# Kernel optimization log

Hardware: AMD Instinct MI355X
Metric: run time of the kernel (lower is better)

Reference implementation:

```python
import jax, jax.numpy as jnp
import numpy as np

NEG = -10000.0
T, K = 65536, 512


def setup_inputs() -> dict:
    key = jax.random.key(0)
    k1, k2 = jax.random.split(key)
    feats = jax.random.normal(k1, (T, K), dtype=jnp.float32)
    transitions = jax.random.normal(k2, (K, K), dtype=jnp.float32)
    # constraints from __init__: never transition INTO start tag (col 0),
    # never transition OUT of stop tag row (row 1)
    transitions = transitions.at[:, 0].set(NEG).at[1, :].set(NEG)
    return {"feats": feats, "transitions": transitions}


def reference(feats, transitions):
    K_ = transitions.shape[0]
    init = jnp.full((K_,), NEG, dtype=feats.dtype).at[0].set(0.0)

    def step(fv, feat):
        # scores[next, prev] = fv[prev] + transitions[next, prev]
        scores = fv[None, :] + transitions
        bp = jnp.argmax(scores, axis=1).astype(jnp.int32)   # backpointers [K]
        fv_new = jnp.max(scores, axis=1) + feat             # viterbi vars + emission
        return fv_new, bp

    fv, bptrs = jax.lax.scan(step, init, feats)  # bptrs: [T, K]

    terminal = fv + transitions[1]
    best = jnp.argmax(terminal).astype(jnp.int32)
    path_score = terminal[best]

    # backtrack: outs[t] = bptrs[t][path[t]] = path[t-1]; outs[0] is the start tag (0)
    def back(tag, bp):
        nt = bp[tag]
        return nt, nt

    _, outs = jax.lax.scan(back, best, bptrs, reverse=True)
    best_path = jnp.concatenate([outs[1:], best[None]])  # [T], tags per timestep
    return path_score, best_path
```

## Files before the change

### kernel.cpp

```cpp
#include <hip/hip_runtime.h>
#include <cstdint>
#include <cstddef>

#define TT 65536
#define KK 512
#define NEGV (-10000.0f)
#define SEG 256
#define NSEG 256

typedef unsigned short u16;
typedef unsigned int   u32;
typedef unsigned long long u64;

__device__ __forceinline__ float u2f(u32 b){ union{u32 u; float f;} x; x.u=b; return x.f; }
__device__ __forceinline__ u32 f2u(float f){ union{u32 u; float f;} x; x.f=f; return x.u; }

__global__ __launch_bounds__(512)
void sort_rows(const float* __restrict__ trans, u64* __restrict__ svpT,
               u64* __restrict__ svpR)
{
    __shared__ u64 s[KK];
    const int n = blockIdx.x, i = threadIdx.x;
    float x = trans[n*KK + i];
    u32 b = f2u(x);
    u32 ord = (b & 0x80000000u) ? ~b : (b | 0x80000000u);
    s[i] = ((u64)(~ord) << 16) | (u32)i;
    __syncthreads();
    for (int k = 2; k <= KK; k <<= 1){
        for (int j = k >> 1; j > 0; j >>= 1){
            int ixj = i ^ j;
            if (ixj > i){
                u64 a = s[i], c = s[ixj];
                bool up = ((i & k) == 0);
                if ((a > c) == up){ s[i] = c; s[ixj] = a; }
            }
            __syncthreads();
        }
    }
    u64 key = s[i];
    u32 p    = (u32)(key & 0xFFFFu);
    u32 ordv = ~(u32)(key >> 16);
    u32 bits = (ordv & 0x80000000u) ? (ordv ^ 0x80000000u) : ~ordv;
    u64 ent = ((u64)p << 32) | bits;
    svpT[(size_t)i*KK + n] = ent;
    svpR[(size_t)n*KK + i] = ent;
}

__global__ __launch_bounds__(512)
void transpose_k(const float* __restrict__ t, float* __restrict__ tt)
{
    const int c = blockIdx.x, r = threadIdx.x;
    tt[(size_t)c*KK + r] = t[(size_t)r*KK + c];
}

__global__ __launch_bounds__(512)
void fv_scan(const float* __restrict__ feats,
             const u64* __restrict__ svpT,
             const u64* __restrict__ svpR,
             const float* __restrict__ transT,
             float* __restrict__ fvBound,
             float* __restrict__ fmArr,
             float* __restrict__ outScore, int* __restrict__ bestOut)
{
    __shared__ float fvb[2][KK];
    __shared__ float wmaxS[2][8];
    __shared__ u64  bmS[4][8];
    __shared__ u32  cntS[4][8];
    __shared__ u64  bandE[KK + 8];
    __shared__ float rv[KK];
    __shared__ int   ri[KK];

    const int i = threadIdx.x, lane = i & 63, wv = i >> 6;
    const u64 laneLT = (1ull << lane) - 1ull;

    float cV[16]; int cP[16];
#pragma unroll
    for (int k = 0; k < 16; ++k){
        u64 e = svpT[(size_t)k*KK + i];
        cV[k] = u2f((u32)e); cP[k] = (int)(e >> 32);
    }

    float fv_i = fmaxf(NEGV, NEGV + cV[0]) + feats[i];
    fvBound[i] = fv_i;
    float featCur = feats[(size_t)KK + i];

#define VMAX8(k0) { \
    float f0=fvc[cP[k0]],     f1=fvc[cP[(k0)+1]], f2=fvc[cP[(k0)+2]], f3=fvc[cP[(k0)+3]]; \
    float f4=fvc[cP[(k0)+4]], f5=fvc[cP[(k0)+5]], f6=fvc[cP[(k0)+6]], f7=fvc[cP[(k0)+7]]; \
    float m0=fmaxf(f0+cV[k0],     f1+cV[(k0)+1]), m1=fmaxf(f2+cV[(k0)+2], f3+cV[(k0)+3]); \
    float m2=fmaxf(f4+cV[(k0)+4], f5+cV[(k0)+5]), m3=fmaxf(f6+cV[(k0)+6], f7+cV[(k0)+7]); \
    best = fmaxf(best, fmaxf(fmaxf(m0,m1), fmaxf(m2,m3))); }

    for (int t = 1; t < TT; ++t){
        const int cur = t & 1;

        fvb[cur][i] = fv_i;
        float wm = fv_i;
#pragma unroll
        for (int o = 32; o > 0; o >>= 1) wm = fmaxf(wm, __shfl_xor(wm, o, 64));
        if (lane == 0) wmaxS[cur][wv] = wm;
        __syncthreads();
        float fm = wmaxS[cur][0];
#pragma unroll
        for (int w = 1; w < 8; ++w) fm = fmaxf(fm, wmaxS[cur][w]);
        if (i == 0) fmArr[t] = fm;
        const float e0 = fm-0.5f, e1 = fm-1.0f, e2 = fm-1.5f, e3 = fm-2.0f;
        u64 q0 = __ballot(fv_i > e0), q1 = __ballot(fv_i > e1);
        u64 q2 = __ballot(fv_i > e2), q3 = __ballot(fv_i > e3);
        if (lane == 0){
            u64 b0 = q0, b1 = q1&~q0, b2 = q2&~q1, b3 = q3&~q2;
            bmS[0][wv]=b0; cntS[0][wv]=(u32)__builtin_popcountll(b0);
            bmS[1][wv]=b1; cntS[1][wv]=(u32)__builtin_popcountll(b1);
            bmS[2][wv]=b2; cntS[2][wv]=(u32)__builtin_popcountll(b2);
            bmS[3][wv]=b3; cntS[3][wv]=(u32)__builtin_popcountll(b3);
        }

        const float* fvc = fvb[cur];
        float featNxt = __builtin_nontemporal_load(
            &feats[(size_t)(t+1 < TT ? t+1 : t)*KK + i]);
        float best = -3.0e38f;
        VMAX8(0) VMAX8(8)
        __syncthreads();

        u32 tot0=0, tot1=0, tot2=0, tot3=0;
#pragma unroll
        for (int w = 0; w < 8; ++w){
            tot0 += cntS[0][w]; tot1 += cntS[1][w];
            tot2 += cntS[2][w]; tot3 += cntS[3][w];
        }
        int b_i = (fv_i > e0) ? 0 : (fv_i > e1) ? 1 : (fv_i > e2) ? 2 :
                  (fv_i > e3) ? 3 : 4;
        if (b_i < 4){
            u32 off = (b_i > 0 ? tot0 : 0u) + (b_i > 1 ? tot1 : 0u) +
                      (b_i > 2 ? tot2 : 0u);
#pragma unroll
            for (int w = 0; w < 8; ++w) off += (w < wv) ? cntS[b_i][w] : 0u;
            off += (u32)__builtin_popcountll(bmS[b_i][wv] & laneLT);
            bandE[off] = ((u64)f2u(fv_i) << 32) | (u32)i;
        }
        u32 totAll = tot0 + tot1 + tot2 + tot3;
        if (i < 8) bandE[totAll + i] = ((u64)f2u(-1.0e30f) << 32);
        int s0 = __builtin_amdgcn_readfirstlane((int)tot0);
        int s1 = __builtin_amdgcn_readfirstlane((int)tot1);
        int s2 = __builtin_amdgcn_readfirstlane((int)tot2);
        int s3 = __builtin_amdgcn_readfirstlane((int)tot3);
        __syncthreads();

        bool done = false;
        int base = 0;
#pragma unroll
        for (int b = 0; b < 4; ++b){
            const int  cntb = (b==0)?s0:(b==1)?s1:(b==2)?s2:s3;
            const float edge = (b==0)?e0:(b==1)?e1:(b==2)?e2:e3;
            if (__any(!done)){
                if (!done && cntb > 0){
                    for (int u = 0; u < cntb; u += 8){
                        const int jj = base + u;
                        u64 E0=bandE[jj],   E1=bandE[jj+1], E2=bandE[jj+2], E3=bandE[jj+3];
                        u64 E4=bandE[jj+4], E5=bandE[jj+5], E6=bandE[jj+6], E7=bandE[jj+7];
                        int p0=(int)(E0&0xFFFFu), p1=(int)(E1&0xFFFFu);
                        int p2=(int)(E2&0xFFFFu), p3=(int)(E3&0xFFFFu);
                        int p4=(int)(E4&0xFFFFu), p5=(int)(E5&0xFFFFu);
                        int p6=(int)(E6&0xFFFFu), p7=(int)(E7&0xFFFFu);
                        float t0=transT[(size_t)p0*KK+i], t1=transT[(size_t)p1*KK+i];
                        float t2=transT[(size_t)p2*KK+i], t3=transT[(size_t)p3*KK+i];
                        float t4=transT[(size_t)p4*KK+i], t5=transT[(size_t)p5*KK+i];
                        float t6=transT[(size_t)p6*KK+i], t7=transT[(size_t)p7*KK+i];
                        float a0=u2f((u32)(E0>>32))+t0, a1=u2f((u32)(E1>>32))+t1;
                        float a2=u2f((u32)(E2>>32))+t2, a3=u2f((u32)(E3>>32))+t3;
                        float a4=u2f((u32)(E4>>32))+t4, a5=u2f((u32)(E5>>32))+t5;
                        float a6=u2f((u32)(E6>>32))+t6, a7=u2f((u32)(E7>>32))+t7;
                        best = fmaxf(best,
                               fmaxf(fmaxf(fmaxf(a0,a1),fmaxf(a2,a3)),
                                     fmaxf(fmaxf(a4,a5),fmaxf(a6,a7))));
                    }
                }
                done = done || (edge + cV[15] <= best);
            }
            base += cntb;
        }

        u64 pend = __ballot(!done);
        while (pend){
            int r = (int)__ffsll((unsigned long long)pend) - 1;
            pend &= pend - 1;
            const int row = (wv << 6) + r;
            float bestR = __shfl(best, r, 64);
            int rk = 16 + lane;
            for (;;){
                float vv = -1.0e30f, sc = -1.0e30f;
                if (rk < KK){
                    u64 e = svpR[(size_t)row*KK + rk];
                    vv = u2f((u32)e);
                    sc = fvc[(int)(e >> 32)] + vv;
                }
                float m = sc;
#pragma unroll
                for (int o = 32; o > 0; o >>= 1) m = fmaxf(m, __shfl_xor(m, o, 64));
                bestR = fmaxf(bestR, m);
                float vl = __shfl(vv, 63, 64);
                if (e3 + vl <= bestR) break;
                rk += 64;
            }
            if (lane == r) best = bestR;
        }

        fv_i = best + featCur;
        featCur = featNxt;
        if ((t & (SEG-1)) == 0)
            fvBound[(size_t)(t >> 8)*KK + i] = fv_i;
    }
#undef VMAX8

    float tv = fv_i + NEGV;
    rv[i] = tv; ri[i] = i;
    __syncthreads();
    for (int s2 = 256; s2 > 0; s2 >>= 1){
        if (i < s2){
            float v2 = rv[i+s2]; int i2 = ri[i+s2];
            if (v2 > rv[i] || (v2 == rv[i] && i2 < ri[i])){ rv[i] = v2; ri[i] = i2; }
        }
        __syncthreads();
    }
    if (i == 0){ outScore[0] = rv[0]; *bestOut = ri[0]; }
}

__global__ __launch_bounds__(512)
void bp_fill(const float* __restrict__ feats,
             const u64* __restrict__ svpT,
             const float* __restrict__ fvBound,
             const float* __restrict__ fmArr,
             u16* __restrict__ bp)
{
    __shared__ float fvb[2][KK];
    __shared__ u64  r1S[2][8];
    const int i = threadIdx.x, lane = i & 63, wv = i >> 6;
    const int s = blockIdx.x;
    const int t0 = s*SEG + 1;
    const int tEnd = (s == NSEG-1) ? (TT-1) : (s*SEG + SEG);

    float fv_i = fvBound[(size_t)s*KK + i];
    float featC = feats[(size_t)t0*KK + i];

#define TAKE(p_, val_) { float _val=(val_); int _p=(p_); \
    bool _tk = (_val > best) || (_val == best && _p < barg); \
    best = _tk ? _val : best; barg = _tk ? _p : barg; }

    for (int t = t0; t <= tEnd; ++t){
        const int cur = t & 1;
        fvb[cur][i] = fv_i;
        float sc1 = fv_i + NEGV;
        u32 bb = f2u(sc1);
        u32 od = (bb & 0x80000000u) ? ~bb : (bb | 0x80000000u);
        u64 key = ((u64)od << 32) | (u32)(KK - 1 - i);
#pragma unroll
        for (int o = 32; o > 0; o >>= 1){
            u64 ok = __shfl_xor(key, o, 64);
            key = (ok > key) ? ok : key;
        }
        if (lane == 0) r1S[cur][wv] = key;
        float featN = (t < tEnd) ? feats[(size_t)(t+1)*KK + i] : 0.0f;
        __syncthreads();
        const float fm = fmArr[t];
        const float* fvc = fvb[cur];
        float best; int barg;
        if (i == 1){
            u64 kk = r1S[cur][0];
#pragma unroll
            for (int w = 1; w < 8; ++w){ u64 o2 = r1S[cur][w]; kk = (o2 > kk) ? o2 : kk; }
            barg = (KK - 1) - (int)(u32)kk;
            best = fm + NEGV;
        } else {
            best = -3.0e38f; barg = 0;
            for (int kb = 0; kb < KK; kb += 8){
                const u64* sp = &svpT[(size_t)kb*KK + i];
                u64 E0 = sp[0];          u64 E1 = sp[(size_t)KK];
                u64 E2 = sp[(size_t)2*KK]; u64 E3 = sp[(size_t)3*KK];
                u64 E4 = sp[(size_t)4*KK]; u64 E5 = sp[(size_t)5*KK];
                u64 E6 = sp[(size_t)6*KK]; u64 E7 = sp[(size_t)7*KK];
                int p0=(int)(E0>>32), p1=(int)(E1>>32), p2=(int)(E2>>32), p3=(int)(E3>>32);
                int p4=(int)(E4>>32), p5=(int)(E5>>32), p6=(int)(E6>>32), p7=(int)(E7>>32);
                TAKE(p0, fvc[p0] + u2f((u32)E0)); TAKE(p1, fvc[p1] + u2f((u32)E1));
                TAKE(p2, fvc[p2] + u2f((u32)E2)); TAKE(p3, fvc[p3] + u2f((u32)E3));
                TAKE(p4, fvc[p4] + u2f((u32)E4)); TAKE(p5, fvc[p5] + u2f((u32)E5));
                TAKE(p6, fvc[p6] + u2f((u32)E6)); TAKE(p7, fvc[p7] + u2f((u32)E7));
                float vlast = u2f((u32)E7);
                if (fm + vlast < best) break;
            }
        }
        __builtin_nontemporal_store((u16)barg, &bp[(size_t)t*KK + i]);
        fv_i = best + featC;
        featC = featN;
    }
#undef TAKE
}

__global__ __launch_bounds__(512)
void bt_maps(const u16* __restrict__ bp, u16* __restrict__ maps)
{
    const int s = blockIdx.x, e = threadIdx.x;
    const int tEnd = (s == NSEG-1) ? (TT-1) : (s+1)*SEG;
    const int tLow = s*SEG;
    int cur = e;
    for (int t = tEnd; t > tLow; --t) cur = (int)bp[(size_t)t*KK + cur];
    maps[s*KK + e] = (u16)cur;
}

__global__ void bt_boundaries(const u16* __restrict__ maps, const int* __restrict__ bestP,
                              int* __restrict__ btag)
{
    if (threadIdx.x != 0 || blockIdx.x != 0) return;
    int cur = *bestP;
    for (int s = NSEG-1; s >= 0; --s){
        cur = (int)maps[s*KK + cur];
        btag[s] = cur;
    }
}

__global__ void bt_decode(const u16* __restrict__ bp, const int* __restrict__ btag,
                          const int* __restrict__ bestP, float* __restrict__ outPath)
{
    const int s = blockIdx.x;
    if (threadIdx.x != 0) return;
    int tEnd, cur;
    if (s == NSEG-1){ tEnd = TT-1; cur = *bestP; outPath[TT-1] = (float)cur; }
    else            { tEnd = (s+1)*SEG; cur = btag[s+1]; }
    for (int t = tEnd; t > s*SEG; --t){
        cur = (int)bp[(size_t)t*KK + cur];
        outPath[t-1] = (float)cur;
    }
}

extern "C" void kernel_launch(void* const* d_in, const int* in_sizes, int n_in,
                              void* d_out, int out_size, void* d_ws, size_t ws_size,
                              hipStream_t stream)
{
    (void)in_sizes; (void)n_in; (void)out_size; (void)ws_size;
    const float* feats = (const float*)d_in[0];
    const float* trans = (const float*)d_in[1];
    float* out = (float*)d_out;

    char* ws = (char*)d_ws;
    size_t off = 0;
    u16*   bp     = (u16*)(ws + off);   off += (size_t)TT*KK*sizeof(u16);
    u64*   svpT   = (u64*)(ws + off);   off += (size_t)KK*KK*sizeof(u64);
    u64*   svpR   = (u64*)(ws + off);   off += (size_t)KK*KK*sizeof(u64);
    float* transT = (float*)(ws + off); off += (size_t)KK*KK*sizeof(float);
    float* fvBound= (float*)(ws + off); off += (size_t)NSEG*KK*sizeof(float);
    float* fmArr  = (float*)(ws + off); off += (size_t)TT*sizeof(float);
    u16*   maps   = (u16*)(ws + off);   off += (size_t)NSEG*KK*sizeof(u16);
    int*   btag   = (int*)(ws + off);   off += (size_t)(NSEG+8)*sizeof(int);
    int*   bestP  = (int*)(ws + off);

    hipLaunchKernelGGL(sort_rows,     dim3(KK),   dim3(512), 0, stream, trans, svpT, svpR);
    hipLaunchKernelGGL(transpose_k,   dim3(KK),   dim3(512), 0, stream, trans, transT);
    hipLaunchKernelGGL(fv_scan,       dim3(1),    dim3(512), 0, stream, feats, svpT, svpR,
                       transT, fvBound, fmArr, out, bestP);
    hipLaunchKernelGGL(bp_fill,       dim3(NSEG), dim3(512), 0, stream, feats, svpT,
                       fvBound, fmArr, bp);
    hipLaunchKernelGGL(bt_maps,       dim3(NSEG), dim3(512), 0, stream, bp, maps);
    hipLaunchKernelGGL(bt_boundaries, dim3(1),    dim3(64),  0, stream, maps, bestP, btag);
    hipLaunchKernelGGL(bt_decode,     dim3(NSEG), dim3(64),  0, stream, bp, btag, bestP, out + 1);
}
```

Measured before the change: 297.4 ms.

## Replace band compaction with per-wave bitmask iteration and add argmax-candidate seeding

Drops the shared-memory prefix-sum compaction of band candidates and the extra barrier it needed. Each band is now walked directly from per-wave ballot bitmasks using ffs. The band count grows from four to eight, widening the pruning range before falling back to the slow sorted-row scan. Each wave's argmax previous state (packed into a 64-bit key) is also used to seed the running best with its transition column, which tightens the early-exit bound. The costs are serialized bitmask loops with scalar readfirstlane, eight extra global loads of transT per step, and possibly more band iterations.

```diff
diff --git a/kernel.cpp b/kernel.cpp
--- a/kernel.cpp
+++ b/kernel.cpp
@@ -63,15 +63,12 @@
              float* __restrict__ outScore, int* __restrict__ bestOut)
 {
     __shared__ float fvb[2][KK];
-    __shared__ float wmaxS[2][8];
-    __shared__ u64  bmS[4][8];
-    __shared__ u32  cntS[4][8];
-    __shared__ u64  bandE[KK + 8];
+    __shared__ u64  wmaxS[2][8];
+    __shared__ u64  bmS[8][8];
     __shared__ float rv[KK];
     __shared__ int   ri[KK];
 
     const int i = threadIdx.x, lane = i & 63, wv = i >> 6;
-    const u64 laneLT = (1ull << lane) - 1ull;
 
     float cV[16]; int cP[16];
 #pragma unroll
@@ -79,6 +76,7 @@
         u64 e = svpT[(size_t)k*KK + i];
         cV[k] = u2f((u32)e); cP[k] = (int)(e >> 32);
     }
+    const float cv15 = cV[15];
 
     float fv_i = fmaxf(NEGV, NEGV + cV[0]) + feats[i];
     fvBound[i] = fv_i;
@@ -95,24 +93,48 @@
         const int cur = t & 1;
 
         fvb[cur][i] = fv_i;
-        float wm = fv_i;
-#pragma unroll
-        for (int o = 32; o > 0; o >>= 1) wm = fmaxf(wm, __shfl_xor(wm, o, 64));
-        if (lane == 0) wmaxS[cur][wv] = wm;
+        {
+            u32 ob = f2u(fv_i);
+            ob = (ob & 0x80000000u) ? ~ob : (ob | 0x80000000u);
+            u64 key = ((u64)ob << 32) | (u32)i;
+#pragma unroll
+            for (int o = 32; o > 0; o >>= 1){
+                u64 ok = __shfl_xor(key, o, 64);
+                key = (ok > key) ? ok : key;
+            }
+            if (lane == 0) wmaxS[cur][wv] = key;
+        }
         __syncthreads();
-        float fm = wmaxS[cur][0];
-#pragma unroll
-        for (int w = 1; w < 8; ++w) fm = fmaxf(fm, wmaxS[cur][w]);
+
+        float wmv[8], pfv[8];
+#pragma unroll
+        for (int w = 0; w < 8; ++w){
+            u64 kw = wmaxS[cur][w];
+            u32 ov = (u32)(kw >> 32);
+            u32 bits = (ov & 0x80000000u) ? (ov ^ 0x80000000u) : ~ov;
+            wmv[w] = u2f(bits);
+            int pw = __builtin_amdgcn_readfirstlane((int)(u32)kw);
+            pfv[w] = transT[(size_t)pw*KK + i];
+        }
+        float fm = wmv[0];
+#pragma unroll
+        for (int w = 1; w < 8; ++w) fm = fmaxf(fm, wmv[w]);
         if (i == 0) fmArr[t] = fm;
+
         const float e0 = fm-0.5f, e1 = fm-1.0f, e2 = fm-1.5f, e3 = fm-2.0f;
-        u64 q0 = __ballot(fv_i > e0), q1 = __ballot(fv_i > e1);
-        u64 q2 = __ballot(fv_i > e2), q3 = __ballot(fv_i > e3);
-        if (lane == 0){
-            u64 b0 = q0, b1 = q1&~q0, b2 = q2&~q1, b3 = q3&~q2;
-            bmS[0][wv]=b0; cntS[0][wv]=(u32)__builtin_popcountll(b0);
-            bmS[1][wv]=b1; cntS[1][wv]=(u32)__builtin_popcountll(b1);
-            bmS[2][wv]=b2; cntS[2][wv]=(u32)__builtin_popcountll(b2);
-            bmS[3][wv]=b3; cntS[3][wv]=(u32)__builtin_popcountll(b3);
+        const float e4 = fm-2.5f, e5 = fm-3.0f, e6 = fm-3.5f, e7 = fm-4.0f;
+        {
+            u64 q0 = __ballot(fv_i > e0), q1 = __ballot(fv_i > e1);
+            u64 q2 = __ballot(fv_i > e2), q3 = __ballot(fv_i > e3);
+            u64 q4 = __ballot(fv_i > e4), q5 = __ballot(fv_i > e5);
+            u64 q6 = __ballot(fv_i > e6), q7 = __ballot(fv_i > e7);
+            if (lane < 8){
+                u64 mb = (lane==0)? q0      : (lane==1)? (q1&~q0) :
+                         (lane==2)? (q2&~q1): (lane==3)? (q3&~q2) :
+                         (lane==4)? (q4&~q3): (lane==5)? (q5&~q4) :
+                         (lane==6)? (q6&~q5):            (q7&~q6);
+                bmS[lane][wv] = mb;
+            }
         }
 
         const float* fvc = fvb[cur];
@@ -120,64 +142,41 @@
             &feats[(size_t)(t+1 < TT ? t+1 : t)*KK + i]);
         float best = -3.0e38f;
         VMAX8(0) VMAX8(8)
+#pragma unroll
+        for (int w = 0; w < 8; ++w) best = fmaxf(best, wmv[w] + pfv[w]);
         __syncthreads();
 
-        u32 tot0=0, tot1=0, tot2=0, tot3=0;
-#pragma unroll
-        for (int w = 0; w < 8; ++w){
-            tot0 += cntS[0][w]; tot1 += cntS[1][w];
-            tot2 += cntS[2][w]; tot3 += cntS[3][w];
-        }
-        int b_i = (fv_i > e0) ? 0 : (fv_i > e1) ? 1 : (fv_i > e2) ? 2 :
-                  (fv_i > e3) ? 3 : 4;
-        if (b_i < 4){
-            u32 off = (b_i > 0 ? tot0 : 0u) + (b_i > 1 ? tot1 : 0u) +
-                      (b_i > 2 ? tot2 : 0u);
-#pragma unroll
-            for (int w = 0; w < 8; ++w) off += (w < wv) ? cntS[b_i][w] : 0u;
-            off += (u32)__builtin_popcountll(bmS[b_i][wv] & laneLT);
-            bandE[off] = ((u64)f2u(fv_i) << 32) | (u32)i;
-        }
-        u32 totAll = tot0 + tot1 + tot2 + tot3;
-        if (i < 8) bandE[totAll + i] = ((u64)f2u(-1.0e30f) << 32);
-        int s0 = __builtin_amdgcn_readfirstlane((int)tot0);
-        int s1 = __builtin_amdgcn_readfirstlane((int)tot1);
-        int s2 = __builtin_amdgcn_readfirstlane((int)tot2);
-        int s3 = __builtin_amdgcn_readfirstlane((int)tot3);
-        __syncthreads();
-
         bool done = false;
-        int base = 0;
-#pragma unroll
-        for (int b = 0; b < 4; ++b){
-            const int  cntb = (b==0)?s0:(b==1)?s1:(b==2)?s2:s3;
-            const float edge = (b==0)?e0:(b==1)?e1:(b==2)?e2:e3;
-            if (__any(!done)){
-                if (!done && cntb > 0){
-                    for (int u = 0; u < cntb; u += 8){
-                        const int jj = base + u;
-                        u64 E0=bandE[jj],   E1=bandE[jj+1], E2=bandE[jj+2], E3=bandE[jj+3];
-                        u64 E4=bandE[jj+4], E5=bandE[jj+5], E6=bandE[jj+6], E7=bandE[jj+7];
-                        int p0=(int)(E0&0xFFFFu), p1=(int)(E1&0xFFFFu);
-                        int p2=(int)(E2&0xFFFFu), p3=(int)(E3&0xFFFFu);
-                        int p4=(int)(E4&0xFFFFu), p5=(int)(E5&0xFFFFu);
-                        int p6=(int)(E6&0xFFFFu), p7=(int)(E7&0xFFFFu);
-                        float t0=transT[(size_t)p0*KK+i], t1=transT[(size_t)p1*KK+i];
-                        float t2=transT[(size_t)p2*KK+i], t3=transT[(size_t)p3*KK+i];
-                        float t4=transT[(size_t)p4*KK+i], t5=transT[(size_t)p5*KK+i];
-                        float t6=transT[(size_t)p6*KK+i], t7=transT[(size_t)p7*KK+i];
-                        float a0=u2f((u32)(E0>>32))+t0, a1=u2f((u32)(E1>>32))+t1;
-                        float a2=u2f((u32)(E2>>32))+t2, a3=u2f((u32)(E3>>32))+t3;
-                        float a4=u2f((u32)(E4>>32))+t4, a5=u2f((u32)(E5>>32))+t5;
-                        float a6=u2f((u32)(E6>>32))+t6, a7=u2f((u32)(E7>>32))+t7;
-                        best = fmaxf(best,
-                               fmaxf(fmaxf(fmaxf(a0,a1),fmaxf(a2,a3)),
-                                     fmaxf(fmaxf(a4,a5),fmaxf(a6,a7))));
+#pragma unroll 1
+        for (int b = 0; b < 8; ++b){
+            if (!__any(!done)) break;
+            const float edge = fm - 0.5f*(float)(b+1);
+            if (!done){
+#pragma unroll 1
+                for (int w = 0; w < 8; ++w){
+                    u64 mraw = bmS[b][w];
+                    u32 mlo = __builtin_amdgcn_readfirstlane((u32)mraw);
+                    u32 mhi = __builtin_amdgcn_readfirstlane((u32)(mraw >> 32));
+                    u64 m = ((u64)mhi << 32) | mlo;
+                    const int pb0 = w << 6;
+                    while (m){
+                        int a0 = (int)__ffsll(m) - 1;  u64 mm = m & (m-1);
+                        int a1 = mm ? (int)__ffsll(mm)-1 : a0;  mm &= (mm-1);
+                        int a2 = mm ? (int)__ffsll(mm)-1 : a0;  mm &= (mm-1);
+                        int a3 = mm ? (int)__ffsll(mm)-1 : a0;  mm &= (mm-1);
+                        m = mm;
+                        const int P0 = pb0+a0, P1 = pb0+a1, P2 = pb0+a2, P3 = pb0+a3;
+                        float f0 = fvc[P0], f1 = fvc[P1], f2 = fvc[P2], f3 = fvc[P3];
+                        float t0 = transT[(size_t)P0*KK + i];
+                        float t1 = transT[(size_t)P1*KK + i];
+                        float t2 = transT[(size_t)P2*KK + i];
+                        float t3 = transT[(size_t)P3*KK + i];
+                        best = fmaxf(best, fmaxf(fmaxf(f0+t0, f1+t1),
+                                                 fmaxf(f2+t2, f3+t3)));
                     }
                 }
-                done = done || (edge + cV[15] <= best);
-            }
-            base += cntb;
+                done = (edge + cv15 <= best);
+            }
         }
 
         u64 pend = __ballot(!done);
@@ -199,7 +198,7 @@
                 for (int o = 32; o > 0; o >>= 1) m = fmaxf(m, __shfl_xor(m, o, 64));
                 bestR = fmaxf(bestR, m);
                 float vl = __shfl(vv, 63, 64);
-                if (e3 + vl <= bestR) break;
+                if (e7 + vl <= bestR) break;
                 rk += 64;
             }
             if (lane == r) best = bestR;
```

Result: slower. 636.6 ms (+114.0%).
